# Kernel optimization log

Hardware: AMD Instinct MI355X
Metric: run time of the kernel (lower is better)

The kernel has to match this reference:

```python
import jax, jax.numpy as jnp
import numpy as np

B, C, H, W = 8, 512, 64, 64
CQ = C // 8  # query/key projection dim


def setup_inputs() -> dict:
    key = jax.random.key(0)
    ks = jax.random.split(key, 8)
    s = 0.02
    return {
        "x": jax.random.normal(ks[0], (B, C, H, W), dtype=jnp.float32),
        "Wq": jax.random.normal(ks[1], (CQ, C), dtype=jnp.float32) * s,
        "bq": jax.random.normal(ks[2], (CQ,), dtype=jnp.float32) * s,
        "Wk": jax.random.normal(ks[3], (CQ, C), dtype=jnp.float32) * s,
        "bk": jax.random.normal(ks[4], (CQ,), dtype=jnp.float32) * s,
        "Wv": jax.random.normal(ks[5], (C, C), dtype=jnp.float32) * s,
        "bv": jax.random.normal(ks[6], (C,), dtype=jnp.float32) * s,
        "gamma": jax.random.normal(ks[7], (1,), dtype=jnp.float32) * 0.1,
    }


def reference(x, Wq, bq, Wk, bk, Wv, bv, gamma):
    b, c, h, w = x.shape
    n = h * w
    xf = x.reshape(b, c, n)                                  # [B,C,N]
    # 1x1 convs == per-pixel linear maps over channels
    q = jnp.einsum('dc,bcn->bdn', Wq, xf) + bq[:, None]       # [B,CQ,N]
    k = jnp.einsum('dc,bcn->bdn', Wk, xf) + bk[:, None]       # [B,CQ,N]
    v = jnp.einsum('dc,bcn->bdn', Wv, xf) + bv[:, None]       # [B,C,N]
    # attention[b, i, j] = softmax_j( q_i . k_j )
    attn = jax.nn.softmax(jnp.einsum('bdn,bdm->bnm', q, k), axis=-1)  # [B,N,N]
    # out[b, c, i] = sum_j v[b, c, j] * attn[b, i, j]
    out = jnp.einsum('bcj,bij->bci', v, attn).reshape(b, c, h, w)
    return gamma[0] * out + x
```

## Files before the change

kernel.cpp:

```cpp
#include <hip/hip_runtime.h>
#include <hip/hip_bf16.h>

#define BB 8
#define CC 512
#define NN 4096
#define CQ 64

typedef __bf16 bf16;
typedef __bf16 bf16x4 __attribute__((ext_vector_type(4)));
typedef __bf16 bf16x8 __attribute__((ext_vector_type(8)));
typedef float f32x4 __attribute__((ext_vector_type(4)));

__device__ __forceinline__ f32x4 mfma16(bf16x8 a, bf16x8 b, f32x4 c) {
    return __builtin_amdgcn_mfma_f32_16x16x32_bf16(a, b, c, 0, 0, 0);
}

#define BAR_LDS()                                            \
    do {                                                     \
        asm volatile("s_waitcnt lgkmcnt(0)" ::: "memory");   \
        __builtin_amdgcn_s_barrier();                        \
    } while (0)


__global__ __launch_bounds__(256) void k_castw(const float* __restrict__ Wq,
                                               const float* __restrict__ Wk,
                                               const float* __restrict__ Wv,
                                               bf16* __restrict__ Wqt,
                                               bf16* __restrict__ Wkt,
                                               bf16* __restrict__ Wvt) {
    int i = blockIdx.x * 256 + threadIdx.x;
    const int nqk = CQ * CC;
    const float* src;
    bf16* dst;
    int j;
    if (i < nqk) {
        src = Wq; dst = Wqt; j = i;
    } else if (i < 2 * nqk) {
        src = Wk; dst = Wkt; j = i - nqk;
    } else if (i < 2 * nqk + CC * CC) {
        src = Wv; dst = Wvt; j = i - 2 * nqk;
    } else {
        return;
    }
    int d = j >> 9;
    int c = j & 511;
    size_t off = ((size_t)(d >> 4) * 16 + (c >> 5)) * 512 + (d & 15) * 32 + (c & 31);
    dst[off] = (bf16)src[j];
}

__global__ __launch_bounds__(256, 2) void k_projf(const float* __restrict__ x,
                                                  const bf16* __restrict__ Wvt,
                                                  const bf16* __restrict__ Wqt,
                                                  const bf16* __restrict__ Wkt,
                                                  const float* __restrict__ bv,
                                                  const float* __restrict__ bq,
                                                  const float* __restrict__ bk,
                                                  bf16* __restrict__ vt,
                                                  bf16* __restrict__ qTt,
                                                  bf16* __restrict__ kTt) {
    __shared__ bf16 XT[2][64][40];

    const int b  = blockIdx.y;
    const int bx = blockIdx.x;
    const int w  = threadIdx.x >> 6;
    const int l  = threadIdx.x & 63;
    const int l15 = l & 15, lq = l >> 4;
    const int loff = l15 * 32 + lq * 8;

    const float* xb = x + (size_t)b * CC * NN + bx * 64 + l;

    f32x4 acc[8][4];
#pragma unroll
    for (int dt = 0; dt < 8; ++dt) {
        f32x4 binit;
#pragma unroll
        for (int r = 0; r < 4; ++r) binit[r] = bv[(w * 8 + dt) * 16 + lq * 4 + r];
#pragma unroll
        for (int nt = 0; nt < 4; ++nt) acc[dt][nt] = binit;
    }
    f32x4 aq[4], ak[4];
    {
        float bvq = bq[w * 16 + l15];
        float bvk = bk[w * 16 + l15];
#pragma unroll
        for (int nt = 0; nt < 4; ++nt) {
            aq[nt] = (f32x4){bvq, bvq, bvq, bvq};
            ak[nt] = (f32x4){bvk, bvk, bvk, bvk};
        }
    }

    auto LOADC = [&](int ct) {
        bf16x8 pk;
#pragma unroll
        for (int r = 0; r < 8; ++r)
            pk[r] = (bf16)xb[(size_t)(ct * 32 + w * 8 + r) * NN];
        return pk;
    };

    {
        bf16x8 c0 = LOADC(0);
        *(bf16x8*)&XT[0][l][w * 8] = c0;
    }
    bf16x8 cnxt = LOADC(1);
    BAR_LDS();

#pragma unroll 2
    for (int ct = 0; ct < 16; ++ct) {
        const int buf = ct & 1;

        bf16x8 c2;
        if (ct < 14) c2 = LOADC(ct + 2);

        bf16x8 bxf[4];
#pragma unroll
        for (int nt = 0; nt < 4; ++nt)
            bxf[nt] = *(const bf16x8*)&XT[buf][nt * 16 + l15][lq * 8];

#pragma unroll
        for (int dt = 0; dt < 8; ++dt) {
            bf16x8 aW = *(const bf16x8*)(Wvt + ((size_t)(w * 8 + dt) * 16 + ct) * 512 + loff);
#pragma unroll
            for (int nt = 0; nt < 4; ++nt)
                acc[dt][nt] = mfma16(aW, bxf[nt], acc[dt][nt]);
        }
        {
            bf16x8 fq = *(const bf16x8*)(Wqt + ((size_t)w * 16 + ct) * 512 + loff);
            bf16x8 fk = *(const bf16x8*)(Wkt + ((size_t)w * 16 + ct) * 512 + loff);
#pragma unroll
            for (int nt = 0; nt < 4; ++nt) {
                aq[nt] = mfma16(bxf[nt], fq, aq[nt]);
                ak[nt] = mfma16(bxf[nt], fk, ak[nt]);
            }
        }

        if (ct < 15)
            *(bf16x8*)&XT[buf ^ 1][l][w * 8] = cnxt;
        cnxt = c2;

        BAR_LDS();
    }

#pragma unroll
    for (int dt = 0; dt < 8; ++dt) {
#pragma unroll
        for (int nt = 0; nt < 4; ++nt) {
#pragma unroll
            for (int r = 0; r < 4; ++r) {
                size_t off = ((size_t)(b * 32 + w * 8 + dt) * 128 + bx * 2 + (nt >> 1)) * 512
                           + (lq * 4 + r) * 32 + (nt & 1) * 16 + l15;
                vt[off] = (bf16)acc[dt][nt][r];
            }
        }
    }
#pragma unroll
    for (int nt = 0; nt < 4; ++nt) {
#pragma unroll
        for (int r = 0; r < 4; ++r) {
            size_t off = ((size_t)(b * 256 + bx * 4 + nt) * 2 + (w >> 1)) * 512
                       + (lq * 4 + r) * 32 + (w & 1) * 16 + l15;
            qTt[off] = (bf16)aq[nt][r];
            kTt[off] = (bf16)ak[nt][r];
        }
    }
}

__global__ __launch_bounds__(512, 2) void k_attn(const bf16* __restrict__ qTt,
                                                 const bf16* __restrict__ kTt,
                                                 const bf16* __restrict__ vt,
                                                 const float* __restrict__ x,
                                                 const float* __restrict__ gamma,
                                                 float* __restrict__ out) {
    __shared__ bf16  Pl[2][8][1024];
    __shared__ bf16  Kl[2][8][512];
    __shared__ float Ll[8][16];

    const int b  = blockIdx.x & 7;
    const int i0 = (blockIdx.x >> 3) * 128;
    const int t  = threadIdx.x;
    const int w  = t >> 6;
    const int l  = t & 63;
    const int l15 = l & 15, lq = l >> 4;
    const int loff = l15 * 32 + lq * 8;

    const f32x4 zero4 = {0.f, 0.f, 0.f, 0.f};

    const bf16* kb = kTt + (size_t)b * 256 * 2 * 512;
    const bf16* qb = qTt + (size_t)b * 256 * 2 * 512;
    const bf16* vb = vt + ((size_t)b * 32 + w * 4) * 128 * 512 + loff;

    bf16x8 qa0, qa1;
    {
        const bf16* qp = qb + ((size_t)((i0 >> 4) + w) * 2) * 512 + loff;
        qa0 = *(const bf16x8*)qp;
        qa1 = *(const bf16x8*)(qp + 512);
    }

    f32x4 acc[4][8];
#pragma unroll
    for (int ct = 0; ct < 4; ++ct)
#pragma unroll
        for (int it = 0; it < 8; ++it) acc[ct][it] = zero4;
    float lsum = 0.f;

    bf16x8 kcur;
    {
        bf16x8 k0 = *(const bf16x8*)(kb + (size_t)w * 512 + loff);
        *(bf16x8*)&Kl[0][w][l * 8] = k0;
        kcur = *(const bf16x8*)(kb + (size_t)(8 + w) * 512 + loff);
    }
    BAR_LDS();

#pragma unroll 2
    for (int jb = 0; jb < NN / 64; ++jb) {
        const int buf = jb & 1;

        bf16x8 va[4][2];
#pragma unroll
        for (int ct = 0; ct < 4; ++ct)
#pragma unroll
            for (int h = 0; h < 2; ++h)
                va[ct][h] = *(const bf16x8*)(vb + ((size_t)ct * 128 + jb * 2 + h) * 512);

        bf16x8 knxt;
        {
            const int jk = (jb + 2) & (NN / 64 - 1);
            knxt = *(const bf16x8*)(kb + ((size_t)jk * 8 + w) * 512 + loff);
        }

        bf16x8 ka[8];
#pragma unroll
        for (int q = 0; q < 8; ++q)
            ka[q] = *(const bf16x8*)&Kl[buf][q][l * 8];

        f32x4 st[4];
#pragma unroll
        for (int jt = 0; jt < 4; ++jt) {
            f32x4 s = mfma16(ka[jt * 2], qa0, zero4);
            st[jt] = mfma16(ka[jt * 2 + 1], qa1, s);
        }

        *(bf16x8*)&Kl[buf ^ 1][w][l * 8] = kcur;
        kcur = knxt;

#pragma unroll
        for (int jt = 0; jt < 4; ++jt) {
            float p0 = __expf(st[jt][0]);
            float p1 = __expf(st[jt][1]);
            float p2 = __expf(st[jt][2]);
            float p3 = __expf(st[jt][3]);
            lsum += (p0 + p1) + (p2 + p3);
            bf16x4 pk = {(bf16)p0, (bf16)p1, (bf16)p2, (bf16)p3};
            int g = jt * 2 + (lq >> 1);
            *(bf16x4*)&Pl[buf][w][g * 128 + l15 * 8 + (lq & 1) * 4] = pk;
        }

        BAR_LDS();

        __builtin_amdgcn_s_setprio(1);
        bf16x8 pA = *(const bf16x8*)&Pl[buf][0][l * 8];
        bf16x8 pB = *(const bf16x8*)&Pl[buf][0][512 + l * 8];
#pragma unroll
        for (int it = 0; it < 8; ++it) {
            bf16x8 nA, nB;
            if (it < 7) {
                nA = *(const bf16x8*)&Pl[buf][it + 1][l * 8];
                nB = *(const bf16x8*)&Pl[buf][it + 1][512 + l * 8];
            }
            acc[0][it] = mfma16(va[0][0], pA, acc[0][it]);
            acc[1][it] = mfma16(va[1][0], pA, acc[1][it]);
            acc[2][it] = mfma16(va[2][0], pA, acc[2][it]);
            acc[3][it] = mfma16(va[3][0], pA, acc[3][it]);
            acc[0][it] = mfma16(va[0][1], pB, acc[0][it]);
            acc[1][it] = mfma16(va[1][1], pB, acc[1][it]);
            acc[2][it] = mfma16(va[2][1], pB, acc[2][it]);
            acc[3][it] = mfma16(va[3][1], pB, acc[3][it]);
            pA = nA;
            pB = nB;
        }
        __builtin_amdgcn_s_setprio(0);
    }

    lsum += __shfl_xor(lsum, 16);
    lsum += __shfl_xor(lsum, 32);
    if (l < 16) Ll[w][l] = lsum;
    __syncthreads();

    const float g = gamma[0];
    float linv[8];
#pragma unroll
    for (int it = 0; it < 8; ++it) linv[it] = 1.0f / Ll[it][l15];

#pragma unroll
    for (int ct = 0; ct < 4; ++ct) {
#pragma unroll
        for (int it = 0; it < 8; ++it) {
#pragma unroll
            for (int r = 0; r < 4; ++r) {
                int c = (w * 4 + ct) * 16 + lq * 4 + r;
                size_t idx = ((size_t)b * CC + c) * NN + i0 + it * 16 + l15;
                out[idx] = g * (acc[ct][it][r] * linv[it]) + x[idx];
            }
        }
    }
}

extern "C" void kernel_launch(void* const* d_in, const int* in_sizes, int n_in,
                              void* d_out, int out_size, void* d_ws, size_t ws_size,
                              hipStream_t stream) {
    const float* x     = (const float*)d_in[0];
    const float* Wq    = (const float*)d_in[1];
    const float* bq    = (const float*)d_in[2];
    const float* Wk    = (const float*)d_in[3];
    const float* bk    = (const float*)d_in[4];
    const float* Wv    = (const float*)d_in[5];
    const float* bv    = (const float*)d_in[6];
    const float* gamma = (const float*)d_in[7];
    float* out = (float*)d_out;

    char* p = (char*)d_ws;
    bf16* qTt = (bf16*)p; p += (size_t)BB * NN * CQ * sizeof(bf16);
    bf16* kTt = (bf16*)p; p += (size_t)BB * NN * CQ * sizeof(bf16);
    bf16* vt  = (bf16*)p; p += (size_t)BB * CC * NN * sizeof(bf16);
    bf16* Wqt = (bf16*)p; p += (size_t)CQ * CC * sizeof(bf16);
    bf16* Wkt = (bf16*)p; p += (size_t)CQ * CC * sizeof(bf16);
    bf16* Wvt = (bf16*)p; p += (size_t)CC * CC * sizeof(bf16);

    k_castw<<<(2 * CQ * CC + CC * CC + 255) / 256, 256, 0, stream>>>(Wq, Wk, Wv, Wqt, Wkt, Wvt);
    k_projf<<<dim3(NN / 64, BB), 256, 0, stream>>>(x, Wvt, Wqt, Wkt, bv, bq, bk, vt, qTt, kTt);
    k_attn<<<256, 512, 0, stream>>>(qTt, kTt, vt, x, gamma, out);
}
```

Baseline: 188.1 us.

## Process 128 keys per iteration to halve barriers in attention loop

```diff
diff --git a/kernel.cpp b/kernel.cpp
--- a/kernel.cpp
+++ b/kernel.cpp
@@ -170,8 +170,8 @@
                                                  const float* __restrict__ x,
                                                  const float* __restrict__ gamma,
                                                  float* __restrict__ out) {
-    __shared__ bf16  Pl[2][8][1024];
-    __shared__ bf16  Kl[2][8][512];
+    __shared__ bf16  Pl[2][8][2048];
+    __shared__ bf16  Kl[2][16][512];
     __shared__ float Ll[8][16];
 
     const int b  = blockIdx.x & 7;
@@ -202,48 +202,55 @@
         for (int it = 0; it < 8; ++it) acc[ct][it] = zero4;
     float lsum = 0.f;
 
-    bf16x8 kcur;
     {
-        bf16x8 k0 = *(const bf16x8*)(kb + (size_t)w * 512 + loff);
-        *(bf16x8*)&Kl[0][w][l * 8] = k0;
-        kcur = *(const bf16x8*)(kb + (size_t)(8 + w) * 512 + loff);
+        bf16x8 k0a = *(const bf16x8*)(kb + (size_t)w * 512 + loff);
+        bf16x8 k0b = *(const bf16x8*)(kb + (size_t)(w + 8) * 512 + loff);
+        *(bf16x8*)&Kl[0][w][l * 8]     = k0a;
+        *(bf16x8*)&Kl[0][w + 8][l * 8] = k0b;
     }
     BAR_LDS();
 
-#pragma unroll 2
-    for (int jb = 0; jb < NN / 64; ++jb) {
+#pragma unroll 1
+    for (int jb = 0; jb < NN / 128; ++jb) {
         const int buf = jb & 1;
 
-        bf16x8 va[4][2];
+        bf16x8 kc0, kc1;
+        {
+            const int jn = (jb + 1) & (NN / 128 - 1);
+            kc0 = *(const bf16x8*)(kb + ((size_t)jn * 16 + w) * 512 + loff);
+            kc1 = *(const bf16x8*)(kb + ((size_t)jn * 16 + w + 8) * 512 + loff);
+        }
+
+        f32x4 st[8];
+        {
+            bf16x8 ka[8];
+#pragma unroll
+            for (int q = 0; q < 8; ++q)
+                ka[q] = *(const bf16x8*)&Kl[buf][q][l * 8];
+#pragma unroll
+            for (int jt = 0; jt < 4; ++jt) {
+                f32x4 s = mfma16(ka[jt * 2], qa0, zero4);
+                st[jt] = mfma16(ka[jt * 2 + 1], qa1, s);
+            }
+#pragma unroll
+            for (int q = 0; q < 8; ++q)
+                ka[q] = *(const bf16x8*)&Kl[buf][8 + q][l * 8];
+#pragma unroll
+            for (int jt = 0; jt < 4; ++jt) {
+                f32x4 s = mfma16(ka[jt * 2], qa0, zero4);
+                st[4 + jt] = mfma16(ka[jt * 2 + 1], qa1, s);
+            }
+        }
+
+        bf16x8 vaa[4][2];
 #pragma unroll
         for (int ct = 0; ct < 4; ++ct)
 #pragma unroll
             for (int h = 0; h < 2; ++h)
-                va[ct][h] = *(const bf16x8*)(vb + ((size_t)ct * 128 + jb * 2 + h) * 512);
-
-        bf16x8 knxt;
-        {
-            const int jk = (jb + 2) & (NN / 64 - 1);
-            knxt = *(const bf16x8*)(kb + ((size_t)jk * 8 + w) * 512 + loff);
-        }
-
-        bf16x8 ka[8];
-#pragma unroll
-        for (int q = 0; q < 8; ++q)
-            ka[q] = *(const bf16x8*)&Kl[buf][q][l * 8];
-
-        f32x4 st[4];
-#pragma unroll
-        for (int jt = 0; jt < 4; ++jt) {
-            f32x4 s = mfma16(ka[jt * 2], qa0, zero4);
-            st[jt] = mfma16(ka[jt * 2 + 1], qa1, s);
-        }
-
-        *(bf16x8*)&Kl[buf ^ 1][w][l * 8] = kcur;
-        kcur = knxt;
-
-#pragma unroll
-        for (int jt = 0; jt < 4; ++jt) {
+                vaa[ct][h] = *(const bf16x8*)(vb + ((size_t)ct * 128 + jb * 4 + h) * 512);
+
+#pragma unroll
+        for (int jt = 0; jt < 8; ++jt) {
             float p0 = __expf(st[jt][0]);
             float p1 = __expf(st[jt][1]);
             float p2 = __expf(st[jt][2]);
@@ -254,28 +261,62 @@
             *(bf16x4*)&Pl[buf][w][g * 128 + l15 * 8 + (lq & 1) * 4] = pk;
         }
 
+        *(bf16x8*)&Kl[buf ^ 1][w][l * 8]     = kc0;
+        *(bf16x8*)&Kl[buf ^ 1][w + 8][l * 8] = kc1;
+
         BAR_LDS();
 
+        bf16x8 vab[4][2];
+#pragma unroll
+        for (int ct = 0; ct < 4; ++ct)
+#pragma unroll
+            for (int h = 0; h < 2; ++h)
+                vab[ct][h] = *(const bf16x8*)(vb + ((size_t)ct * 128 + jb * 4 + 2 + h) * 512);
+
         __builtin_amdgcn_s_setprio(1);
-        bf16x8 pA = *(const bf16x8*)&Pl[buf][0][l * 8];
-        bf16x8 pB = *(const bf16x8*)&Pl[buf][0][512 + l * 8];
-#pragma unroll
-        for (int it = 0; it < 8; ++it) {
-            bf16x8 nA, nB;
-            if (it < 7) {
-                nA = *(const bf16x8*)&Pl[buf][it + 1][l * 8];
-                nB = *(const bf16x8*)&Pl[buf][it + 1][512 + l * 8];
-            }
-            acc[0][it] = mfma16(va[0][0], pA, acc[0][it]);
-            acc[1][it] = mfma16(va[1][0], pA, acc[1][it]);
-            acc[2][it] = mfma16(va[2][0], pA, acc[2][it]);
-            acc[3][it] = mfma16(va[3][0], pA, acc[3][it]);
-            acc[0][it] = mfma16(va[0][1], pB, acc[0][it]);
-            acc[1][it] = mfma16(va[1][1], pB, acc[1][it]);
-            acc[2][it] = mfma16(va[2][1], pB, acc[2][it]);
-            acc[3][it] = mfma16(va[3][1], pB, acc[3][it]);
-            pA = nA;
-            pB = nB;
+        {
+            bf16x8 pA = *(const bf16x8*)&Pl[buf][0][l * 8];
+            bf16x8 pB = *(const bf16x8*)&Pl[buf][0][512 + l * 8];
+#pragma unroll
+            for (int it = 0; it < 8; ++it) {
+                bf16x8 nA, nB;
+                if (it < 7) {
+                    nA = *(const bf16x8*)&Pl[buf][it + 1][l * 8];
+                    nB = *(const bf16x8*)&Pl[buf][it + 1][512 + l * 8];
+                }
+                acc[0][it] = mfma16(vaa[0][0], pA, acc[0][it]);
+                acc[1][it] = mfma16(vaa[1][0], pA, acc[1][it]);
+                acc[2][it] = mfma16(vaa[2][0], pA, acc[2][it]);
+                acc[3][it] = mfma16(vaa[3][0], pA, acc[3][it]);
+                acc[0][it] = mfma16(vaa[0][1], pB, acc[0][it]);
+                acc[1][it] = mfma16(vaa[1][1], pB, acc[1][it]);
+                acc[2][it] = mfma16(vaa[2][1], pB, acc[2][it]);
+                acc[3][it] = mfma16(vaa[3][1], pB, acc[3][it]);
+                pA = nA;
+                pB = nB;
+            }
+        }
+        {
+            bf16x8 pA = *(const bf16x8*)&Pl[buf][0][1024 + l * 8];
+            bf16x8 pB = *(const bf16x8*)&Pl[buf][0][1536 + l * 8];
+#pragma unroll
+            for (int it = 0; it < 8; ++it) {
+                bf16x8 nA, nB;
+                if (it < 7) {
+                    nA = *(const bf16x8*)&Pl[buf][it + 1][1024 + l * 8];
+                    nB = *(const bf16x8*)&Pl[buf][it + 1][1536 + l * 8];
+                }
+                acc[0][it] = mfma16(vab[0][0], pA, acc[0][it]);
+                acc[1][it] = mfma16(vab[1][0], pA, acc[1][it]);
+                acc[2][it] = mfma16(vab[2][0], pA, acc[2][it]);
+                acc[3][it] = mfma16(vab[3][0], pA, acc[3][it]);
+                acc[0][it] = mfma16(vab[0][1], pB, acc[0][it]);
+                acc[1][it] = mfma16(vab[1][1], pB, acc[1][it]);
+                acc[2][it] = mfma16(vab[2][1], pB, acc[2][it]);
+                acc[3][it] = mfma16(vab[3][1], pB, acc[3][it]);
+                pA = nA;
+                pB = nB;
+            }
         }
         __builtin_amdgcn_s_setprio(0);
     }
```

Measured after the change: 216.9 us. +15.3%, slower.

## Switch PV accumulation to 32x32x16 MFMA with retiled V and P layouts

Applied to the files above, without the earlier changes.

```diff
diff --git a/kernel.cpp b/kernel.cpp
--- a/kernel.cpp
+++ b/kernel.cpp
@@ -10,9 +10,13 @@
 typedef __bf16 bf16x4 __attribute__((ext_vector_type(4)));
 typedef __bf16 bf16x8 __attribute__((ext_vector_type(8)));
 typedef float f32x4 __attribute__((ext_vector_type(4)));
+typedef float f32x16 __attribute__((ext_vector_type(16)));
 
 __device__ __forceinline__ f32x4 mfma16(bf16x8 a, bf16x8 b, f32x4 c) {
     return __builtin_amdgcn_mfma_f32_16x16x32_bf16(a, b, c, 0, 0, 0);
+}
+__device__ __forceinline__ f32x16 mfma32(bf16x8 a, bf16x8 b, f32x16 c) {
+    return __builtin_amdgcn_mfma_f32_32x32x16_bf16(a, b, c, 0, 0, 0);
 }
 
 #define BAR_LDS()                                            \
@@ -146,8 +150,10 @@
         for (int nt = 0; nt < 4; ++nt) {
 #pragma unroll
             for (int r = 0; r < 4; ++r) {
-                size_t off = ((size_t)(b * 32 + w * 8 + dt) * 128 + bx * 2 + (nt >> 1)) * 512
-                           + (lq * 4 + r) * 32 + (nt & 1) * 16 + l15;
+                int c = (w * 8 + dt) * 16 + lq * 4 + r;
+                int n = bx * 64 + nt * 16 + l15;
+                size_t off = (((size_t)b * 16 + (c >> 5)) * 256 + (n >> 4)) * 512
+                           + (c & 31) * 16 + (n & 15);
                 vt[off] = (bf16)acc[dt][nt][r];
             }
         }
@@ -170,9 +176,9 @@
                                                  const float* __restrict__ x,
                                                  const float* __restrict__ gamma,
                                                  float* __restrict__ out) {
-    __shared__ bf16  Pl[2][8][1024];
+    __shared__ bf16  Pl[2][128][72];
     __shared__ bf16  Kl[2][8][512];
-    __shared__ float Ll[8][16];
+    __shared__ float Ll[128];
 
     const int b  = blockIdx.x & 7;
     const int i0 = (blockIdx.x >> 3) * 128;
@@ -180,13 +186,15 @@
     const int w  = t >> 6;
     const int l  = t & 63;
     const int l15 = l & 15, lq = l >> 4;
+    const int l31 = l & 31, lh = l >> 5;
     const int loff = l15 * 32 + lq * 8;
+    const int vloff = l31 * 16 + lh * 8;
 
     const f32x4 zero4 = {0.f, 0.f, 0.f, 0.f};
 
     const bf16* kb = kTt + (size_t)b * 256 * 2 * 512;
     const bf16* qb = qTt + (size_t)b * 256 * 2 * 512;
-    const bf16* vb = vt + ((size_t)b * 32 + w * 4) * 128 * 512 + loff;
+    const bf16* vb = vt + (size_t)b * 16 * 256 * 512 + vloff;
 
     bf16x8 qa0, qa1;
     {
@@ -195,11 +203,16 @@
         qa1 = *(const bf16x8*)(qp + 512);
     }
 
-    f32x4 acc[4][8];
-#pragma unroll
-    for (int ct = 0; ct < 4; ++ct)
-#pragma unroll
-        for (int it = 0; it < 8; ++it) acc[ct][it] = zero4;
+    f32x16 acc32[2][4];
+    {
+        f32x16 z;
+#pragma unroll
+        for (int r = 0; r < 16; ++r) z[r] = 0.f;
+#pragma unroll
+        for (int ctt = 0; ctt < 2; ++ctt)
+#pragma unroll
+            for (int it = 0; it < 4; ++it) acc32[ctt][it] = z;
+    }
     float lsum = 0.f;
 
     bf16x8 kcur;
@@ -214,12 +227,13 @@
     for (int jb = 0; jb < NN / 64; ++jb) {
         const int buf = jb & 1;
 
-        bf16x8 va[4][2];
-#pragma unroll
-        for (int ct = 0; ct < 4; ++ct)
-#pragma unroll
-            for (int h = 0; h < 2; ++h)
-                va[ct][h] = *(const bf16x8*)(vb + ((size_t)ct * 128 + jb * 2 + h) * 512);
+        bf16x8 vf[2][4];
+#pragma unroll
+        for (int ctt = 0; ctt < 2; ++ctt)
+#pragma unroll
+            for (int ks = 0; ks < 4; ++ks)
+                vf[ctt][ks] = *(const bf16x8*)(vb
+                    + ((size_t)(w * 2 + ctt) * 256 + jb * 4 + ks) * 512);
 
         bf16x8 knxt;
         {
@@ -250,55 +264,46 @@
             float p3 = __expf(st[jt][3]);
             lsum += (p0 + p1) + (p2 + p3);
             bf16x4 pk = {(bf16)p0, (bf16)p1, (bf16)p2, (bf16)p3};
-            int g = jt * 2 + (lq >> 1);
-            *(bf16x4*)&Pl[buf][w][g * 128 + l15 * 8 + (lq & 1) * 4] = pk;
+            *(bf16x4*)&Pl[buf][w * 16 + l15][jt * 16 + lq * 4] = pk;
         }
 
         BAR_LDS();
 
         __builtin_amdgcn_s_setprio(1);
-        bf16x8 pA = *(const bf16x8*)&Pl[buf][0][l * 8];
-        bf16x8 pB = *(const bf16x8*)&Pl[buf][0][512 + l * 8];
-#pragma unroll
-        for (int it = 0; it < 8; ++it) {
-            bf16x8 nA, nB;
-            if (it < 7) {
-                nA = *(const bf16x8*)&Pl[buf][it + 1][l * 8];
-                nB = *(const bf16x8*)&Pl[buf][it + 1][512 + l * 8];
+#pragma unroll
+        for (int it = 0; it < 4; ++it) {
+            bf16x8 pB[4];
+#pragma unroll
+            for (int ks = 0; ks < 4; ++ks)
+                pB[ks] = *(const bf16x8*)&Pl[buf][it * 32 + l31][ks * 16 + lh * 8];
+#pragma unroll
+            for (int ks = 0; ks < 4; ++ks) {
+                acc32[0][it] = mfma32(vf[0][ks], pB[ks], acc32[0][it]);
+                acc32[1][it] = mfma32(vf[1][ks], pB[ks], acc32[1][it]);
             }
-            acc[0][it] = mfma16(va[0][0], pA, acc[0][it]);
-            acc[1][it] = mfma16(va[1][0], pA, acc[1][it]);
-            acc[2][it] = mfma16(va[2][0], pA, acc[2][it]);
-            acc[3][it] = mfma16(va[3][0], pA, acc[3][it]);
-            acc[0][it] = mfma16(va[0][1], pB, acc[0][it]);
-            acc[1][it] = mfma16(va[1][1], pB, acc[1][it]);
-            acc[2][it] = mfma16(va[2][1], pB, acc[2][it]);
-            acc[3][it] = mfma16(va[3][1], pB, acc[3][it]);
-            pA = nA;
-            pB = nB;
         }
         __builtin_amdgcn_s_setprio(0);
     }
 
     lsum += __shfl_xor(lsum, 16);
     lsum += __shfl_xor(lsum, 32);
-    if (l < 16) Ll[w][l] = lsum;
+    if (l < 16) Ll[w * 16 + l] = lsum;
     __syncthreads();
 
     const float g = gamma[0];
-    float linv[8];
-#pragma unroll
-    for (int it = 0; it < 8; ++it) linv[it] = 1.0f / Ll[it][l15];
-
-#pragma unroll
-    for (int ct = 0; ct < 4; ++ct) {
-#pragma unroll
-        for (int it = 0; it < 8; ++it) {
-#pragma unroll
-            for (int r = 0; r < 4; ++r) {
-                int c = (w * 4 + ct) * 16 + lq * 4 + r;
-                size_t idx = ((size_t)b * CC + c) * NN + i0 + it * 16 + l15;
-                out[idx] = g * (acc[ct][it][r] * linv[it]) + x[idx];
+    float linv[4];
+#pragma unroll
+    for (int it = 0; it < 4; ++it) linv[it] = 1.0f / Ll[it * 32 + l31];
+
+#pragma unroll
+    for (int ctt = 0; ctt < 2; ++ctt) {
+#pragma unroll
+        for (int it = 0; it < 4; ++it) {
+#pragma unroll
+            for (int reg = 0; reg < 16; ++reg) {
+                int c = w * 64 + ctt * 32 + (reg & 3) + 8 * (reg >> 2) + 4 * lh;
+                size_t idx = ((size_t)b * CC + c) * NN + i0 + it * 32 + l31;
+                out[idx] = g * (acc32[ctt][it][reg] * linv[it]) + x[idx];
             }
         }
     }
```

New measurement: 196.3 us. +4.3%, slower.
